# Optimization experiments

Hardware: AMD Instinct MI355X
Metric: run time of the kernel (lower is better)

The kernel has to match this reference:

```python
import jax, jax.numpy as jnp
import numpy as np

B, N, HC, HH, K, D = 64, 300, 64, 64, 3, 10

def setup_inputs() -> dict:
    key = jax.random.key(0)
    ks = jax.random.split(key, 8)
    inp = {
        "z": jax.random.normal(ks[0], (B, N, HC), dtype=jnp.float32),
        "W_in": jax.random.normal(ks[1], (HH, HC), dtype=jnp.float32) / np.sqrt(HC),
        "b_in": jax.random.normal(ks[2], (HH,), dtype=jnp.float32) * 0.01,
        "W_out": jax.random.normal(ks[3], (HC * HC, HH), dtype=jnp.float32) / np.sqrt(HH),
        "b_out": jax.random.normal(ks[4], (HC * HC,), dtype=jnp.float32) * 0.01,
        "node_emb": jax.random.normal(ks[5], (N, D), dtype=jnp.float32),
        "weights_pool": jax.random.normal(ks[6], (D, K, HH, HH), dtype=jnp.float32) / np.sqrt(D * HH),
        "bias_pool": jax.random.normal(ks[7], (D, HH), dtype=jnp.float32) * 0.01,
    }
    return inp

def _agc(z, node_emb, weights_pool, bias_pool):
    n = node_emb.shape[0]
    # data-adaptive adjacency: softmax over rows of relu(E E^T)
    supports = jax.nn.softmax(jax.nn.relu(node_emb @ node_emb.T), axis=1)  # [N,N]
    support_set = [jnp.eye(n, dtype=z.dtype), supports]
    for _ in range(2, K):  # Chebyshev recursion T_k = 2A T_{k-1} - T_{k-2}
        support_set.append(2.0 * supports @ support_set[-1] - support_set[-2])
    S = jnp.stack(support_set, axis=0)  # [K,N,N]
    weights = jnp.einsum('nd,dkio->nkio', node_emb, weights_pool)  # [N,K,HH,HH]
    bias = node_emb @ bias_pool  # [N,HH]
    x_g = jnp.einsum('knm,bmc->bnkc', S, z)  # [B,N,K,HH]
    return jnp.einsum('bnki,nkio->bno', x_g, weights) + bias

def reference(z, W_in, b_in, W_out, b_out, node_emb, weights_pool, bias_pool):
    h = jax.nn.relu(z @ W_in.T + b_in)                  # [B,N,HH]
    h = _agc(h, node_emb, weights_pool, bias_pool)      # [B,N,HH]
    out = (h @ W_out.T + b_out).reshape(B, N, HC, HC)   # [B,N,HC,HC]
    return jnp.tanh(out)
```

## Files before the change

kernel.cpp:

```cpp
#include <hip/hip_runtime.h>
#include <hip/hip_bf16.h>

#define BB 64
#define NN 300
#define HH 64
#define RTOT (BB*NN)
#define KIO  (3*HH*HH)
#define JOUT (HH*HH)

typedef __attribute__((ext_vector_type(8))) _Float16 f16x8;
typedef __attribute__((ext_vector_type(4))) float floatx4;

__device__ inline float tanh_fast(float x) {
    float e = __expf(2.f * x);
    return 1.f - 2.f * __builtin_amdgcn_rcpf(e + 1.f);
}

__global__ __launch_bounds__(256) void k_pre(const float* __restrict__ E,
                                             const float* __restrict__ z,
                                             const float* __restrict__ Win,
                                             const float* __restrict__ bin,
                                             const float* __restrict__ Wout,
                                             const float* __restrict__ bpool,
                                             float* __restrict__ A,
                                             float* __restrict__ h,
                                             float* __restrict__ bN,
                                             _Float16* __restrict__ Wh) {
    __shared__ float smem[8576];
    int bid = blockIdx.x, tid = threadIdx.x;

    if (bid < 300) {
        float* sE  = smem;
        float* row = smem + 16;
        float* red = smem + 320;
        int n = bid;
        if (tid < 10) sE[tid] = E[n*10 + tid];
        __syncthreads();
        float lmax = -1e30f;
        for (int m = tid; m < NN; m += 256) {
            float s = 0.f;
            #pragma unroll
            for (int d = 0; d < 10; ++d) s += sE[d] * E[m*10 + d];
            s = fmaxf(s, 0.f);
            row[m] = s;
            lmax = fmaxf(lmax, s);
        }
        red[tid] = lmax; __syncthreads();
        for (int off = 128; off > 0; off >>= 1) {
            if (tid < off) red[tid] = fmaxf(red[tid], red[tid+off]);
            __syncthreads();
        }
        float mx = red[0]; __syncthreads();
        float lsum = 0.f;
        for (int m = tid; m < NN; m += 256) {
            float e = __expf(row[m] - mx);
            row[m] = e;
            lsum += e;
        }
        red[tid] = lsum; __syncthreads();
        for (int off = 128; off > 0; off >>= 1) {
            if (tid < off) red[tid] += red[tid+off];
            __syncthreads();
        }
        float inv = 1.f / red[0];
        for (int m = tid; m < NN; m += 256) A[n*NN + m] = row[m] * inv;
    } else if (bid < 600) {
        float* Wt = smem;
        float* zl = smem + 4352;
        int tx = tid & 15, ty = tid >> 4;
        int r0 = (bid - 300) * 64;
        for (int e = tid; e < 4096; e += 256) {
            int o = e >> 6, c = e & 63;
            Wt[c*68 + o] = Win[e];
            zl[o*66 + c] = z[(size_t)(r0 + o)*64 + c];
        }
        __syncthreads();
        float4 bo = *(const float4*)&bin[tx*4];
        float acc[4][4];
        #pragma unroll
        for (int s = 0; s < 4; ++s) { acc[s][0]=bo.x; acc[s][1]=bo.y; acc[s][2]=bo.z; acc[s][3]=bo.w; }
        const float* zr = &zl[(ty*4)*66];
        for (int c = 0; c < 64; ++c) {
            float4 w = *(const float4*)&Wt[c*68 + tx*4];
            float z0 = zr[c], z1 = zr[66+c], z2 = zr[132+c], z3 = zr[198+c];
            acc[0][0] += z0*w.x; acc[0][1] += z0*w.y; acc[0][2] += z0*w.z; acc[0][3] += z0*w.w;
            acc[1][0] += z1*w.x; acc[1][1] += z1*w.y; acc[1][2] += z1*w.z; acc[1][3] += z1*w.w;
            acc[2][0] += z2*w.x; acc[2][1] += z2*w.y; acc[2][2] += z2*w.z; acc[2][3] += z2*w.w;
            acc[3][0] += z3*w.x; acc[3][1] += z3*w.y; acc[3][2] += z3*w.z; acc[3][3] += z3*w.w;
        }
        #pragma unroll
        for (int s = 0; s < 4; ++s) {
            float4 v = make_float4(fmaxf(acc[s][0],0.f), fmaxf(acc[s][1],0.f),
                                   fmaxf(acc[s][2],0.f), fmaxf(acc[s][3],0.f));
            *(float4*)&h[(size_t)(r0 + ty*4 + s)*64 + tx*4] = v;
        }
    } else if (bid < 675) {
        int idx = (bid - 600)*256 + tid;
        int n = idx >> 6, o = idx & 63;
        float s = 0.f;
        #pragma unroll
        for (int d = 0; d < 10; ++d) s += E[n*10 + d] * bpool[d*64 + o];
        bN[idx] = s;
    } else {
        int idx = (bid - 675)*256 + tid;
        Wh[idx] = (_Float16)Wout[idx];
    }
}

__global__ __launch_bounds__(256) void k_spatialA(const float* __restrict__ A,
                                                  const float* __restrict__ h,
                                                  float* __restrict__ xg1) {
    int tid = threadIdx.x;
    int c = tid & 63;
    int w = __builtin_amdgcn_readfirstlane(tid >> 6);
    int b = blockIdx.y;
    int r0 = blockIdx.x * 20 + w * 5;
    const float* S = A + (size_t)r0 * NN;
    const float* hb = h + (size_t)b * NN * 64 + c;
    float a0 = 0.f, a1 = 0.f, a2 = 0.f, a3 = 0.f, a4 = 0.f;
    for (int m = 0; m < NN; m += 4) {
        float4 s0 = *(const float4*)(S + 0*NN + m);
        float4 s1 = *(const float4*)(S + 1*NN + m);
        float4 s2 = *(const float4*)(S + 2*NN + m);
        float4 s3 = *(const float4*)(S + 3*NN + m);
        float4 s4 = *(const float4*)(S + 4*NN + m);
        float h0 = hb[(m+0)*64];
        float h1 = hb[(m+1)*64];
        float h2 = hb[(m+2)*64];
        float h3 = hb[(m+3)*64];
        a0 = fmaf(s0.x,h0,a0); a0 = fmaf(s0.y,h1,a0); a0 = fmaf(s0.z,h2,a0); a0 = fmaf(s0.w,h3,a0);
        a1 = fmaf(s1.x,h0,a1); a1 = fmaf(s1.y,h1,a1); a1 = fmaf(s1.z,h2,a1); a1 = fmaf(s1.w,h3,a1);
        a2 = fmaf(s2.x,h0,a2); a2 = fmaf(s2.y,h1,a2); a2 = fmaf(s2.z,h2,a2); a2 = fmaf(s2.w,h3,a2);
        a3 = fmaf(s3.x,h0,a3); a3 = fmaf(s3.y,h1,a3); a3 = fmaf(s3.z,h2,a3); a3 = fmaf(s3.w,h3,a3);
        a4 = fmaf(s4.x,h0,a4); a4 = fmaf(s4.y,h1,a4); a4 = fmaf(s4.z,h2,a4); a4 = fmaf(s4.w,h3,a4);
    }
    float* dst = xg1 + ((size_t)b * NN + r0) * 64 + c;
    dst[0*64] = a0; dst[1*64] = a1; dst[2*64] = a2; dst[3*64] = a3; dst[4*64] = a4;
}

__global__ __launch_bounds__(256) void k_spatialB(const float* __restrict__ A,
                                                  const float* __restrict__ xg1,
                                                  const float* __restrict__ h,
                                                  float* __restrict__ xg2) {
    int tid = threadIdx.x;
    int c = tid & 63;
    int w = __builtin_amdgcn_readfirstlane(tid >> 6);
    int b = blockIdx.y;
    int r0 = blockIdx.x * 20 + w * 5;
    const float* S = A + (size_t)r0 * NN;
    const float* xb = xg1 + (size_t)b * NN * 64 + c;
    float a0 = 0.f, a1 = 0.f, a2 = 0.f, a3 = 0.f, a4 = 0.f;
    for (int m = 0; m < NN; m += 4) {
        float4 s0 = *(const float4*)(S + 0*NN + m);
        float4 s1 = *(const float4*)(S + 1*NN + m);
        float4 s2 = *(const float4*)(S + 2*NN + m);
        float4 s3 = *(const float4*)(S + 3*NN + m);
        float4 s4 = *(const float4*)(S + 4*NN + m);
        float x0 = xb[(m+0)*64];
        float x1 = xb[(m+1)*64];
        float x2 = xb[(m+2)*64];
        float x3 = xb[(m+3)*64];
        a0 = fmaf(s0.x,x0,a0); a0 = fmaf(s0.y,x1,a0); a0 = fmaf(s0.z,x2,a0); a0 = fmaf(s0.w,x3,a0);
        a1 = fmaf(s1.x,x0,a1); a1 = fmaf(s1.y,x1,a1); a1 = fmaf(s1.z,x2,a1); a1 = fmaf(s1.w,x3,a1);
        a2 = fmaf(s2.x,x0,a2); a2 = fmaf(s2.y,x1,a2); a2 = fmaf(s2.z,x2,a2); a2 = fmaf(s2.w,x3,a2);
        a3 = fmaf(s3.x,x0,a3); a3 = fmaf(s3.y,x1,a3); a3 = fmaf(s3.z,x2,a3); a3 = fmaf(s3.w,x3,a3);
        a4 = fmaf(s4.x,x0,a4); a4 = fmaf(s4.y,x1,a4); a4 = fmaf(s4.z,x2,a4); a4 = fmaf(s4.w,x3,a4);
    }
    const float* hb = h   + ((size_t)b * NN + r0) * 64 + c;
    float*       dst = xg2 + ((size_t)b * NN + r0) * 64 + c;
    dst[0*64] = 2.f*a0 - hb[0*64];
    dst[1*64] = 2.f*a1 - hb[1*64];
    dst[2*64] = 2.f*a2 - hb[2*64];
    dst[3*64] = 2.f*a3 - hb[3*64];
    dst[4*64] = 2.f*a4 - hb[4*64];
}

__global__ __launch_bounds__(256) void k_node_mm(const float* __restrict__ h,
                                                 const float* __restrict__ xg1,
                                                 const float* __restrict__ xg2,
                                                 const float* __restrict__ pool,
                                                 const float* __restrict__ E,
                                                 const float* __restrict__ bN,
                                                 _Float16* __restrict__ h2h) {
    __shared__ float Wnl[12288];
    __shared__ float xgl[32][192];
    int tid = threadIdx.x;
    int n = blockIdx.x, b0 = blockIdx.y * 32;

    float Ev[10];
    #pragma unroll
    for (int d = 0; d < 10; ++d) Ev[d] = E[n*10 + d];

    const float4* p4 = (const float4*)pool;
    for (int e4 = tid; e4 < 3072; e4 += 256) {
        float4 acc = make_float4(0.f, 0.f, 0.f, 0.f);
        #pragma unroll
        for (int d = 0; d < 10; ++d) {
            float4 pv = p4[d*3072 + e4];
            acc.x = fmaf(Ev[d], pv.x, acc.x);
            acc.y = fmaf(Ev[d], pv.y, acc.y);
            acc.z = fmaf(Ev[d], pv.z, acc.z);
            acc.w = fmaf(Ev[d], pv.w, acc.w);
        }
        ((float4*)Wnl)[e4] = acc;
    }

    for (int e4 = tid; e4 < 1536; e4 += 256) {
        int gi = e4 * 4;
        int bb = gi / 192, kb = gi % 192;
        int k = kb >> 6, i = kb & 63;
        const float* src = (k == 0) ? h : ((k == 1) ? xg1 : xg2);
        *(float4*)&xgl[bb][kb] = *(const float4*)&src[((size_t)(b0 + bb)*NN + n)*64 + i];
    }
    __syncthreads();

    int o = tid & 63, ty = tid >> 6;
    float bias = bN[n*64 + o];
    for (int bb = ty; bb < 32; bb += 4) {
        float acc = bias;
        for (int ki = 0; ki < 192; ki += 4) {
            float4 x4 = *(const float4*)&xgl[bb][ki];
            float w0 = Wnl[(ki+0)*64 + o];
            float w1 = Wnl[(ki+1)*64 + o];
            float w2 = Wnl[(ki+2)*64 + o];
            float w3 = Wnl[(ki+3)*64 + o];
            acc = fmaf(x4.x, w0, acc); acc = fmaf(x4.y, w1, acc);
            acc = fmaf(x4.z, w2, acc); acc = fmaf(x4.w, w3, acc);
        }
        h2h[((size_t)(b0 + bb)*NN + n)*64 + o] = (_Float16)acc;
    }
}

__global__ __launch_bounds__(256) void k_out_proj_mfma(const _Float16* __restrict__ h2h,
                                                       const _Float16* __restrict__ Wh,
                                                       const float* __restrict__ bout,
                                                       float* __restrict__ out) {
    int tid  = threadIdx.x;
    int wave = tid >> 6, lane = tid & 63;
    int quad = lane >> 4, lr = lane & 15;
    int m0 = blockIdx.y*128 + (wave >> 1)*64;
    int n0 = blockIdx.x*128 + (wave & 1)*64;
    floatx4 acc[4][4] = {};
    const _Float16* Aptr = h2h + (size_t)(m0 + lr)*64 + quad*8;
    const _Float16* Bptr = Wh  + (size_t)(n0 + lr)*64 + quad*8;
    #pragma unroll
    for (int ks = 0; ks < 2; ++ks) {
        f16x8 a[4], b[4];
        #pragma unroll
        for (int f = 0; f < 4; ++f) {
            a[f] = *(const f16x8*)(Aptr + (size_t)f*16*64 + ks*32);
            b[f] = *(const f16x8*)(Bptr + (size_t)f*16*64 + ks*32);
        }
        #pragma unroll
        for (int mf = 0; mf < 4; ++mf)
            #pragma unroll
            for (int nf = 0; nf < 4; ++nf)
                acc[mf][nf] = __builtin_amdgcn_mfma_f32_16x16x32_f16(b[nf], a[mf], acc[mf][nf], 0, 0, 0);
    }
    #pragma unroll
    for (int nf = 0; nf < 4; ++nf) {
        int c0 = n0 + nf*16 + quad*4;
        float4 bj = *(const float4*)&bout[c0];
        #pragma unroll
        for (int mf = 0; mf < 4; ++mf) {
            int row = m0 + mf*16 + lr;
            floatx4 v;
            v[0] = tanh_fast(acc[mf][nf][0] + bj.x);
            v[1] = tanh_fast(acc[mf][nf][1] + bj.y);
            v[2] = tanh_fast(acc[mf][nf][2] + bj.z);
            v[3] = tanh_fast(acc[mf][nf][3] + bj.w);
            __builtin_nontemporal_store(v, (floatx4*)&out[(size_t)row*JOUT + c0]);
        }
    }
}

extern "C" void kernel_launch(void* const* d_in, const int* in_sizes, int n_in,
                              void* d_out, int out_size, void* d_ws, size_t ws_size,
                              hipStream_t stream) {
    const float* z     = (const float*)d_in[0];
    const float* Win   = (const float*)d_in[1];
    const float* bin   = (const float*)d_in[2];
    const float* Wout  = (const float*)d_in[3];
    const float* bout  = (const float*)d_in[4];
    const float* E     = (const float*)d_in[5];
    const float* pool  = (const float*)d_in[6];
    const float* bpool = (const float*)d_in[7];
    float* out = (float*)d_out;

    float* ws  = (float*)d_ws;
    float* A   = ws;
    float* bN  = A   + 90000;
    float* h   = bN  + 19200;
    float* xg1 = h   + 1228800;
    float* xg2 = xg1 + 1228800;
    _Float16* h2h   = (_Float16*)(xg2 + 1228800);
    _Float16* Wouth = h2h + 1228800;

    k_pre      <<<1699, 256, 0, stream>>>(E, z, Win, bin, Wout, bpool,
                                          A, h, bN, Wouth);
    k_spatialA <<<dim3(15, BB), 256, 0, stream>>>(A, h, xg1);
    k_spatialB <<<dim3(15, BB), 256, 0, stream>>>(A, xg1, h, xg2);
    k_node_mm  <<<dim3(NN, 2), 256, 0, stream>>>(h, xg1, xg2, pool, E, bN, h2h);
    k_out_proj_mfma<<<dim3(JOUT/128, RTOT/128), 256, 0, stream>>>(h2h, Wouth, bout, out);
}
```

Measured before the change: 451.7 us.

## Fuse all stages into one persistent cooperative kernel with grid syncs

Replaces the five separate kernel launches with a single cooperative persistent kernel of 512 blocks that loops over each stage's work units and separates stages with grid-wide syncs. The aim is to remove launch gaps and per-launch overhead between the dependent stages. In exchange, each stage now runs on a fixed 512-block grid with one shared 72 KB LDS allocation, which can lower occupancy. The large MFMA output stage loses the scheduling freedom of a full grid. The old kernels remain as a fallback if the cooperative launch fails.

```diff
diff --git a/kernel.cpp b/kernel.cpp
--- a/kernel.cpp
+++ b/kernel.cpp
@@ -1,5 +1,8 @@
 #include <hip/hip_runtime.h>
+#include <hip/hip_cooperative_groups.h>
 #include <hip/hip_bf16.h>
+
+namespace cg = cooperative_groups;
 
 #define BB 64
 #define NN 300
@@ -16,19 +19,13 @@
     return 1.f - 2.f * __builtin_amdgcn_rcpf(e + 1.f);
 }
 
-__global__ __launch_bounds__(256) void k_pre(const float* __restrict__ E,
-                                             const float* __restrict__ z,
-                                             const float* __restrict__ Win,
-                                             const float* __restrict__ bin,
-                                             const float* __restrict__ Wout,
-                                             const float* __restrict__ bpool,
-                                             float* __restrict__ A,
-                                             float* __restrict__ h,
-                                             float* __restrict__ bN,
-                                             _Float16* __restrict__ Wh) {
-    __shared__ float smem[8576];
-    int bid = blockIdx.x, tid = threadIdx.x;
-
+
+__device__ void pre_unit(int bid, int tid, float* smem,
+                         const float* __restrict__ E, const float* __restrict__ z,
+                         const float* __restrict__ Win, const float* __restrict__ bin,
+                         const float* __restrict__ Wout, const float* __restrict__ bpool,
+                         float* __restrict__ A, float* __restrict__ h,
+                         float* __restrict__ bN, _Float16* __restrict__ Wh) {
     if (bid < 300) {
         float* sE  = smem;
         float* row = smem + 16;
@@ -107,14 +104,13 @@
     }
 }
 
-__global__ __launch_bounds__(256) void k_spatialA(const float* __restrict__ A,
-                                                  const float* __restrict__ h,
-                                                  float* __restrict__ xg1) {
-    int tid = threadIdx.x;
+__device__ void spatialA_unit(int u, int tid,
+                              const float* __restrict__ A, const float* __restrict__ h,
+                              float* __restrict__ xg1) {
     int c = tid & 63;
     int w = __builtin_amdgcn_readfirstlane(tid >> 6);
-    int b = blockIdx.y;
-    int r0 = blockIdx.x * 20 + w * 5;
+    int b = u / 15;
+    int r0 = (u % 15) * 20 + w * 5;
     const float* S = A + (size_t)r0 * NN;
     const float* hb = h + (size_t)b * NN * 64 + c;
     float a0 = 0.f, a1 = 0.f, a2 = 0.f, a3 = 0.f, a4 = 0.f;
@@ -138,15 +134,13 @@
     dst[0*64] = a0; dst[1*64] = a1; dst[2*64] = a2; dst[3*64] = a3; dst[4*64] = a4;
 }
 
-__global__ __launch_bounds__(256) void k_spatialB(const float* __restrict__ A,
-                                                  const float* __restrict__ xg1,
-                                                  const float* __restrict__ h,
-                                                  float* __restrict__ xg2) {
-    int tid = threadIdx.x;
+__device__ void spatialB_unit(int u, int tid,
+                              const float* __restrict__ A, const float* __restrict__ xg1,
+                              const float* __restrict__ h, float* __restrict__ xg2) {
     int c = tid & 63;
     int w = __builtin_amdgcn_readfirstlane(tid >> 6);
-    int b = blockIdx.y;
-    int r0 = blockIdx.x * 20 + w * 5;
+    int b = u / 15;
+    int r0 = (u % 15) * 20 + w * 5;
     const float* S = A + (size_t)r0 * NN;
     const float* xb = xg1 + (size_t)b * NN * 64 + c;
     float a0 = 0.f, a1 = 0.f, a2 = 0.f, a3 = 0.f, a4 = 0.f;
@@ -175,17 +169,13 @@
     dst[4*64] = 2.f*a4 - hb[4*64];
 }
 
-__global__ __launch_bounds__(256) void k_node_mm(const float* __restrict__ h,
-                                                 const float* __restrict__ xg1,
-                                                 const float* __restrict__ xg2,
-                                                 const float* __restrict__ pool,
-                                                 const float* __restrict__ E,
-                                                 const float* __restrict__ bN,
-                                                 _Float16* __restrict__ h2h) {
-    __shared__ float Wnl[12288];
-    __shared__ float xgl[32][192];
-    int tid = threadIdx.x;
-    int n = blockIdx.x, b0 = blockIdx.y * 32;
+__device__ void node_unit(int n, int b0, int tid, float* lds,
+                          const float* __restrict__ h, const float* __restrict__ xg1,
+                          const float* __restrict__ xg2, const float* __restrict__ pool,
+                          const float* __restrict__ E, const float* __restrict__ bN,
+                          _Float16* __restrict__ h2h) {
+    float* Wnl = lds;
+    float* xgl = lds + 12288;
 
     float Ev[10];
     #pragma unroll
@@ -210,7 +200,7 @@
         int bb = gi / 192, kb = gi % 192;
         int k = kb >> 6, i = kb & 63;
         const float* src = (k == 0) ? h : ((k == 1) ? xg1 : xg2);
-        *(float4*)&xgl[bb][kb] = *(const float4*)&src[((size_t)(b0 + bb)*NN + n)*64 + i];
+        *(float4*)&xgl[bb*192 + kb] = *(const float4*)&src[((size_t)(b0 + bb)*NN + n)*64 + i];
     }
     __syncthreads();
 
@@ -219,7 +209,7 @@
     for (int bb = ty; bb < 32; bb += 4) {
         float acc = bias;
         for (int ki = 0; ki < 192; ki += 4) {
-            float4 x4 = *(const float4*)&xgl[bb][ki];
+            float4 x4 = *(const float4*)&xgl[bb*192 + ki];
             float w0 = Wnl[(ki+0)*64 + o];
             float w1 = Wnl[(ki+1)*64 + o];
             float w2 = Wnl[(ki+2)*64 + o];
@@ -231,15 +221,13 @@
     }
 }
 
-__global__ __launch_bounds__(256) void k_out_proj_mfma(const _Float16* __restrict__ h2h,
-                                                       const _Float16* __restrict__ Wh,
-                                                       const float* __restrict__ bout,
-                                                       float* __restrict__ out) {
-    int tid  = threadIdx.x;
+__device__ void out_unit(int ux, int uy, int tid,
+                         const _Float16* __restrict__ h2h, const _Float16* __restrict__ Wh,
+                         const float* __restrict__ bout, float* __restrict__ out) {
     int wave = tid >> 6, lane = tid & 63;
     int quad = lane >> 4, lr = lane & 15;
-    int m0 = blockIdx.y*128 + (wave >> 1)*64;
-    int n0 = blockIdx.x*128 + (wave & 1)*64;
+    int m0 = uy*128 + (wave >> 1)*64;
+    int n0 = ux*128 + (wave & 1)*64;
     floatx4 acc[4][4] = {};
     const _Float16* Aptr = h2h + (size_t)(m0 + lr)*64 + quad*8;
     const _Float16* Bptr = Wh  + (size_t)(n0 + lr)*64 + quad*8;
@@ -274,15 +262,92 @@
     }
 }
 
+__global__ __launch_bounds__(256) void k_fused(
+        const float* __restrict__ E, const float* __restrict__ z,
+        const float* __restrict__ Win, const float* __restrict__ bin,
+        const float* __restrict__ Wout, const float* __restrict__ bout,
+        const float* __restrict__ pool, const float* __restrict__ bpool,
+        float* __restrict__ A, float* __restrict__ h, float* __restrict__ bN,
+        float* __restrict__ xg1, float* __restrict__ xg2,
+        _Float16* __restrict__ h2h, _Float16* __restrict__ Wh,
+        float* __restrict__ out) {
+    __shared__ float lds[18432];
+    cg::grid_group grid = cg::this_grid();
+    int bid = blockIdx.x, tid = threadIdx.x;
+    int nblk = gridDim.x;
+
+    for (int u = bid; u < 1699; u += nblk) {
+        __syncthreads();
+        pre_unit(u, tid, lds, E, z, Win, bin, Wout, bpool, A, h, bN, Wh);
+    }
+    grid.sync();
+    for (int u = bid; u < 960; u += nblk) spatialA_unit(u, tid, A, h, xg1);
+    grid.sync();
+    for (int u = bid; u < 960; u += nblk) spatialB_unit(u, tid, A, xg1, h, xg2);
+    grid.sync();
+    for (int u = bid; u < 600; u += nblk) {
+        __syncthreads();
+        node_unit(u % 300, (u / 300) * 32, tid, lds, h, xg1, xg2, pool, E, bN, h2h);
+    }
+    grid.sync();
+    for (int u = bid; u < 4800; u += nblk) out_unit(u % 32, u / 32, tid, h2h, Wh, bout, out);
+}
+
+
+__global__ __launch_bounds__(256) void k_pre(const float* __restrict__ E,
+                                             const float* __restrict__ z,
+                                             const float* __restrict__ Win,
+                                             const float* __restrict__ bin,
+                                             const float* __restrict__ Wout,
+                                             const float* __restrict__ bpool,
+                                             float* __restrict__ A,
+                                             float* __restrict__ h,
+                                             float* __restrict__ bN,
+                                             _Float16* __restrict__ Wh) {
+    __shared__ float smem[8576];
+    pre_unit(blockIdx.x, threadIdx.x, smem, E, z, Win, bin, Wout, bpool, A, h, bN, Wh);
+}
+
+__global__ __launch_bounds__(256) void k_spatialA(const float* __restrict__ A,
+                                                  const float* __restrict__ h,
+                                                  float* __restrict__ xg1) {
+    spatialA_unit(blockIdx.y * 15 + blockIdx.x, threadIdx.x, A, h, xg1);
+}
+
+__global__ __launch_bounds__(256) void k_spatialB(const float* __restrict__ A,
+                                                  const float* __restrict__ xg1,
+                                                  const float* __restrict__ h,
+                                                  float* __restrict__ xg2) {
+    spatialB_unit(blockIdx.y * 15 + blockIdx.x, threadIdx.x, A, xg1, h, xg2);
+}
+
+__global__ __launch_bounds__(256) void k_node_mm(const float* __restrict__ h,
+                                                 const float* __restrict__ xg1,
+                                                 const float* __restrict__ xg2,
+                                                 const float* __restrict__ pool,
+                                                 const float* __restrict__ E,
+                                                 const float* __restrict__ bN,
+                                                 _Float16* __restrict__ h2h) {
+    __shared__ float lds[18432];
+    node_unit(blockIdx.x, blockIdx.y * 32, threadIdx.x, lds, h, xg1, xg2, pool, E, bN, h2h);
+}
+
+__global__ __launch_bounds__(256) void k_out_proj_mfma(const _Float16* __restrict__ h2h,
+                                                       const _Float16* __restrict__ Wh,
+                                                       const float* __restrict__ bout,
+                                                       float* __restrict__ out) {
+    out_unit(blockIdx.x, blockIdx.y, threadIdx.x, h2h, Wh, bout, out);
+}
+
 extern "C" void kernel_launch(void* const* d_in, const int* in_sizes, int n_in,
                               void* d_out, int out_size, void* d_ws, size_t ws_size,
                               hipStream_t stream) {
+    const float* E_    = (const float*)d_in[5];
     const float* z     = (const float*)d_in[0];
     const float* Win   = (const float*)d_in[1];
     const float* bin   = (const float*)d_in[2];
     const float* Wout  = (const float*)d_in[3];
     const float* bout  = (const float*)d_in[4];
-    const float* E     = (const float*)d_in[5];
     const float* pool  = (const float*)d_in[6];
     const float* bpool = (const float*)d_in[7];
     float* out = (float*)d_out;
@@ -296,10 +361,19 @@
     _Float16* h2h   = (_Float16*)(xg2 + 1228800);
     _Float16* Wouth = h2h + 1228800;
 
-    k_pre      <<<1699, 256, 0, stream>>>(E, z, Win, bin, Wout, bpool,
-                                          A, h, bN, Wouth);
-    k_spatialA <<<dim3(15, BB), 256, 0, stream>>>(A, h, xg1);
-    k_spatialB <<<dim3(15, BB), 256, 0, stream>>>(A, xg1, h, xg2);
-    k_node_mm  <<<dim3(NN, 2), 256, 0, stream>>>(h, xg1, xg2, pool, E, bN, h2h);
-    k_out_proj_mfma<<<dim3(JOUT/128, RTOT/128), 256, 0, stream>>>(h2h, Wouth, bout, out);
-}
+    void* args[] = {(void*)&E_, (void*)&z, (void*)&Win, (void*)&bin, (void*)&Wout,
+                    (void*)&bout, (void*)&pool, (void*)&bpool,
+                    (void*)&A, (void*)&h, (void*)&bN, (void*)&xg1, (void*)&xg2,
+                    (void*)&h2h, (void*)&Wouth, (void*)&out};
+    hipError_t err = hipLaunchCooperativeKernel((const void*)k_fused,
+                                                dim3(512), dim3(256),
+                                                args, 0, stream);
+    if (err != hipSuccess) {
+        k_pre      <<<1699, 256, 0, stream>>>(E_, z, Win, bin, Wout, bpool,
+                                              A, h, bN, Wouth);
+        k_spatialA <<<dim3(15, BB), 256, 0, stream>>>(A, h, xg1);
+        k_spatialB <<<dim3(15, BB), 256, 0, stream>>>(A, xg1, h, xg2);
+        k_node_mm  <<<dim3(NN, 2), 256, 0, stream>>>(h, xg1, xg2, pool, E_, bN, h2h);
+        k_out_proj_mfma<<<dim3(JOUT/128, RTOT/128), 256, 0, stream>>>(h2h, Wouth, bout, out);
+    }
+}
```

Result: slower. 741.6 us (+64.2%).
